# Kernel tuning notes

Hardware: AMD Instinct MI355X
Metric: run time of the kernel (lower is better)

Reference implementation:

```python
import jax, jax.numpy as jnp
import numpy as np

B, L, V = 4, 4096, 8192
SIGMA_SCALE = 0.01


def setup_inputs() -> dict:
    key = jax.random.key(0)
    k1, k2, k3, k4 = jax.random.split(key, 4)
    indices = jax.random.randint(k1, (B, L), 0, V, dtype=jnp.int64)
    sigma = jax.random.uniform(k2, (B,), dtype=jnp.float32)
    # nn.Linear(V, V): weight [out=V, in=V], bias [V]
    W = jax.random.normal(k3, (V, V), dtype=jnp.float32) * 0.02
    b = jax.random.normal(k4, (V,), dtype=jnp.float32) * 0.02
    return {"indices": indices, "sigma": sigma, "W": W, "b": b}


def reference(indices, sigma, W, b):
    # Original: logits = Linear(one_hot(clamp(indices)) + 0.01*sigma_effect)
    # one_hot @ W.T  == row-gather of W.T; the sigma term adds a constant
    # c = 0.01*sigma to every vocab slot, contributing c * W.sum(axis=1).
    vocab = W.shape[0]
    idx = jnp.clip(indices, 0, vocab - 1)                 # [B, L]
    gathered = W.T[idx]                                   # [B, L, V] == one_hot @ W.T
    col_sum = jnp.sum(W, axis=1)                          # [V] == (1_V) @ W.T
    sigma_term = (SIGMA_SCALE * sigma)[:, None, None] * col_sum  # [B, L, V]
    logits = gathered + sigma_term + b
    return logits
```

## Files before the change

### kernel.cpp

```cpp
#include <hip/hip_runtime.h>

#define BB 4
#define LL 4096
#define VV 8192
#define NN (BB * LL)
#define SIGMA_SCALE 0.01f

#define CW 64
#define NB (VV / CW)
#define VT 128


__global__ void rowsum_kernel(const float* __restrict__ W,
                              const float* __restrict__ sigma,
                              const float* __restrict__ bias,
                              float* __restrict__ add) {
    __shared__ float red[256];
    const int v = blockIdx.x;
    const float4* row4 = (const float4*)(W + (size_t)v * VV);
    float s = 0.f;
#pragma unroll
    for (int j = threadIdx.x; j < VV / 4; j += 256) {
        float4 x = row4[j];
        s += x.x + x.y + x.z + x.w;
    }
    red[threadIdx.x] = s;
    __syncthreads();
    for (int off = 128; off > 0; off >>= 1) {
        if (threadIdx.x < off) red[threadIdx.x] += red[threadIdx.x + off];
        __syncthreads();
    }
    if (threadIdx.x < BB) {
        add[threadIdx.x * VV + v] =
            SIGMA_SCALE * sigma[threadIdx.x] * red[0] + bias[v];
    }
}

__global__ void bucket_kernel(const int* __restrict__ idx,
                              int* __restrict__ sorted,
                              int* __restrict__ offsets) {
    __shared__ int hist[NB];
    __shared__ int base[NB + 1];
    __shared__ int cursor[NB];
    const int tid = threadIdx.x;
    for (int i = tid; i < NB; i += 256) hist[i] = 0;
    __syncthreads();
    for (int n = tid; n < NN; n += 256) {
        int c = idx[n];
        c = min(max(c, 0), VV - 1);
        atomicAdd(&hist[c >> 6], 1);
    }
    __syncthreads();
    if (tid == 0) {
        int s = 0;
        for (int i = 0; i < NB; ++i) { base[i] = s; s += hist[i]; }
        base[NB] = s;
    }
    __syncthreads();
    for (int i = tid; i <= NB; i += 256) offsets[i] = base[i];
    for (int i = tid; i < NB; i += 256) cursor[i] = 0;
    __syncthreads();
    for (int n = tid; n < NN; n += 256) {
        int c = idx[n];
        c = min(max(c, 0), VV - 1);
        const int bkt = c >> 6;
        const int pos = base[bkt] + atomicAdd(&cursor[bkt], 1);
        sorted[pos] = (n << 13) | c;
    }
}

__global__ __launch_bounds__(256) void gather_fused_kernel(
    const int* __restrict__ sorted, const int* __restrict__ offsets,
    const float* __restrict__ W, const float* __restrict__ add,
    float* __restrict__ out) {
    __shared__ float tile[VT][CW + 1];
    __shared__ float addl[BB][VT];
    const int cb = blockIdx.x;
    const int vb = blockIdx.y;
    const int c0 = cb * CW;
    const int v0 = vb * VT;
    const int tid = threadIdx.x;

    {
        const int r = tid >> 4;
        const int q = tid & 15;
#pragma unroll
        for (int k = 0; k < VT; k += 16) {
            float4 x = *(const float4*)(W + (size_t)(v0 + r + k) * VV + c0 + q * 4);
            tile[r + k][q * 4 + 0] = x.x;
            tile[r + k][q * 4 + 1] = x.y;
            tile[r + k][q * 4 + 2] = x.z;
            tile[r + k][q * 4 + 3] = x.w;
        }
    }
    for (int i = tid; i < BB * VT; i += 256) {
        addl[i / VT][i % VT] = add[(size_t)(i / VT) * VV + v0 + (i % VT)];
    }
    __syncthreads();

    const int start = offsets[cb];
    const int end = offsets[cb + 1];
    const int v = tid & (VT - 1);
    const int which = tid >> 7;
    for (int i = start + which; i < end; i += 2) {
        const int pk = sorted[i];
        const int n = pk >> 13;
        const int cl = (pk & (VV - 1)) - c0;
        const int b = n >> 12;
        out[(size_t)n * VV + v0 + v] = tile[v][cl] + addl[b][v];
    }
}

__global__ void gather_direct_kernel(const int* __restrict__ idx,
                                     const float* __restrict__ W,
                                     const float* __restrict__ add,
                                     float* __restrict__ out) {
    const int n = blockIdx.x;
    const int b = n >> 12;
    int c = idx[n];
    c = min(max(c, 0), VV - 1);
    const int v0 = blockIdx.y * (VV / 4);
    for (int v = v0 + threadIdx.x; v < v0 + VV / 4; v += 256) {
        out[(size_t)n * VV + v] = W[(size_t)v * VV + c] + add[b * VV + v];
    }
}

extern "C" void kernel_launch(void* const* d_in, const int* in_sizes, int n_in,
                              void* d_out, int out_size, void* d_ws,
                              size_t ws_size, hipStream_t stream) {
    const int* indices = (const int*)d_in[0];
    const float* sigma = (const float*)d_in[1];
    const float* W = (const float*)d_in[2];
    const float* bias = (const float*)d_in[3];
    float* out = (float*)d_out;

    float* add = (float*)d_ws;
    const size_t add_bytes = (size_t)BB * VV * sizeof(float);
    int* sorted = (int*)((char*)d_ws + add_bytes);
    const size_t sorted_bytes = (size_t)NN * sizeof(int);
    int* offsets = (int*)((char*)d_ws + add_bytes + sorted_bytes);
    const size_t off_bytes = (size_t)(NB + 1) * sizeof(int);

    rowsum_kernel<<<VV, 256, 0, stream>>>(W, sigma, bias, add);

    if (ws_size >= add_bytes + sorted_bytes + off_bytes) {
        bucket_kernel<<<1, 256, 0, stream>>>(indices, sorted, offsets);
        gather_fused_kernel<<<dim3(NB, VV / VT), 256, 0, stream>>>(
            sorted, offsets, W, add, out);
    } else {
        gather_direct_kernel<<<dim3(NN, 4), 256, 0, stream>>>(indices, W, add, out);
    }
}
```

Before: 812.8 us.

## Transpose shared W tile and emit vectorized nontemporal float4 output stores

The gather kernel now stores the W tile transposed in shared memory, so each output row segment can be read as float4 vectors. Each group of 32 threads writes one 128-float output row slice with 16-byte nontemporal stores, and 8 rows are handled per iteration instead of 2. The aim is to cut store instruction count and write traffic pollution for the large output, which dominates runtime. The transposed tile fill now writes scalar values with strided LDS addresses, which may cause bank conflicts during the load phase.

Measured after the change: 771.0 us. -5.1%, faster.

```diff
diff --git a/kernel.cpp b/kernel.cpp
--- a/kernel.cpp
+++ b/kernel.cpp
@@ -9,6 +9,10 @@
 #define CW 64
 #define NB (VV / CW)
 #define VT 128
+#define VT4 (VT / 4)
+#define VTP (VT4 + 1)
+
+typedef float f4 __attribute__((ext_vector_type(4)));
 
 
 __global__ void rowsum_kernel(const float* __restrict__ W,
@@ -73,8 +77,9 @@
     const int* __restrict__ sorted, const int* __restrict__ offsets,
     const float* __restrict__ W, const float* __restrict__ add,
     float* __restrict__ out) {
-    __shared__ float tile[VT][CW + 1];
-    __shared__ float addl[BB][VT];
+    __shared__ f4 tileT4[CW][VTP];
+    __shared__ f4 addl4[BB][VT4];
+    float* tileT = (float*)tileT4;
     const int cb = blockIdx.x;
     const int vb = blockIdx.y;
     const int c0 = cb * CW;
@@ -86,28 +91,35 @@
         const int q = tid & 15;
 #pragma unroll
         for (int k = 0; k < VT; k += 16) {
-            float4 x = *(const float4*)(W + (size_t)(v0 + r + k) * VV + c0 + q * 4);
-            tile[r + k][q * 4 + 0] = x.x;
-            tile[r + k][q * 4 + 1] = x.y;
-            tile[r + k][q * 4 + 2] = x.z;
-            tile[r + k][q * 4 + 3] = x.w;
+            const int row = r + k;
+            float4 x = *(const float4*)(W + (size_t)(v0 + row) * VV + c0 + q * 4);
+            tileT[(4 * q + 0) * (4 * VTP) + row] = x.x;
+            tileT[(4 * q + 1) * (4 * VTP) + row] = x.y;
+            tileT[(4 * q + 2) * (4 * VTP) + row] = x.z;
+            tileT[(4 * q + 3) * (4 * VTP) + row] = x.w;
         }
     }
-    for (int i = tid; i < BB * VT; i += 256) {
-        addl[i / VT][i % VT] = add[(size_t)(i / VT) * VV + v0 + (i % VT)];
+    if (tid < BB * VT4) {
+        const int b = tid >> 5;
+        const int j = tid & 31;
+        addl4[b][j] = *(const f4*)(add + (size_t)b * VV + v0 + 4 * j);
     }
     __syncthreads();
 
     const int start = offsets[cb];
     const int end = offsets[cb + 1];
-    const int v = tid & (VT - 1);
-    const int which = tid >> 7;
-    for (int i = start + which; i < end; i += 2) {
+    const int slot = tid >> 5;
+    const int j = tid & 31;
+    for (int i = start + slot; i < end; i += 8) {
         const int pk = sorted[i];
         const int n = pk >> 13;
         const int cl = (pk & (VV - 1)) - c0;
         const int b = n >> 12;
-        out[(size_t)n * VV + v0 + v] = tile[v][cl] + addl[b][v];
+        f4 t = tileT4[cl][j];
+        f4 a = addl4[b][j];
+        f4 o = t + a;
+        f4* dst = (f4*)(out + (size_t)n * VV + v0) + j;
+        __builtin_nontemporal_store(o, dst);
     }
 }
 
```
